# Optimization experiments

Hardware: AMD Instinct MI355X
Metric: run time of the kernel (lower is better)

## Reference

```python
import jax, jax.numpy as jnp
import numpy as np

N_NODES = 100000
N_EDGES = 1600000
D = 128


def setup_inputs() -> dict:
    key = jax.random.key(0)
    ks = jax.random.split(key, 8)
    x = jax.random.normal(ks[0], (N_NODES, D), dtype=jnp.float32)
    edge_index = jax.random.randint(ks[1], (2, N_EDGES), 0, N_NODES, dtype=jnp.int64)
    # Linear weights ~ fan-in scaled init
    scale = 1.0 / np.sqrt(D)
    W1 = jax.random.normal(ks[2], (D, D), dtype=jnp.float32) * scale
    W2 = jax.random.normal(ks[3], (D, D), dtype=jnp.float32) * scale
    W3 = jax.random.normal(ks[4], (D, D), dtype=jnp.float32) * scale
    b1 = jnp.zeros((D,), jnp.float32)
    b2 = jnp.zeros((D,), jnp.float32)
    b3 = jnp.zeros((D,), jnp.float32)
    # train_eps=True, PyG initializes eps to 0
    eps1 = jnp.zeros((), jnp.float32)
    eps2 = jnp.zeros((), jnp.float32)
    eps3 = jnp.zeros((), jnp.float32)
    return {"x": x, "edge_index": edge_index,
            "W1": W1, "b1": b1, "eps1": eps1,
            "W2": W2, "b2": b2, "eps2": eps2,
            "W3": W3, "b3": b3, "eps3": eps3}


def _gin_conv(x, src, dst, eps, W, b):
    # scatter-add neighbor aggregation: sum_{j in N(i)} x_j
    agg = jax.ops.segment_sum(x[src], dst, num_segments=N_NODES)  # [N, D]
    h = (1.0 + eps) * x + agg
    return jax.nn.relu(h @ W + b)


def reference(x, edge_index, W1, b1, eps1, W2, b2, eps2, W3, b3, eps3):
    src, dst = edge_index[0], edge_index[1]
    h = _gin_conv(x, src, dst, eps1, W1, b1)   # conv1 (dropout p=0 -> identity)
    h = _gin_conv(h, src, dst, eps2, W2, b2)
    h = _gin_conv(h, src, dst, eps3, W3, b3)
    return jax.nn.log_softmax(h, axis=1)
```

## Files before the change

### kernel.cpp

```cpp
#include <hip/hip_runtime.h>
#include <hip/hip_bf16.h>

#define N_NODES 100000
#define N_EDGES 1600000
#define D 128
#define NRANGE 8
#define RANGE_SZ 12500
#define SB_PER_RANGE 196
#define NBUCKET (NRANGE * SB_PER_RANGE)
#define G_PART 512
#define CH_PART 3125
#define G_DEG 128
#define CH_DEG 784
#define G_X2B 12500
#define PLANE ((size_t)N_NODES * 64)

typedef __attribute__((ext_vector_type(8))) short bf16x8;
typedef __attribute__((ext_vector_type(8))) unsigned short u16x8;
typedef __attribute__((ext_vector_type(4))) float f32x4;
typedef unsigned int u32;

__device__ inline ushort f2b(float x) {
    union { float f; unsigned u; } v; v.f = x;
    unsigned r = (v.u + 0x7fff + ((v.u >> 16) & 1)) >> 16;
    return (ushort)r;
}
__device__ inline float b2f(ushort b) {
    union { unsigned u; float f; } v; v.u = ((unsigned)b) << 16;
    return v.f;
}

__global__ void prep_kernel(const float* __restrict__ x, ushort* __restrict__ xb,
                            const int* __restrict__ dst, int* __restrict__ bhist1,
                            const float* __restrict__ W1, const float* __restrict__ W2,
                            const float* __restrict__ W3,
                            ushort* __restrict__ wt_hi, ushort* __restrict__ wt_lo) {
    __shared__ int lh[NRANGE];
    int b = blockIdx.x;
    if (b < G_X2B) {
        int i = b * 256 + threadIdx.x;
        if (i < N_NODES * D / 4) {
            float4 v = ((const float4*)x)[i];
            ushort4 o;
            o.x = f2b(v.x); o.y = f2b(v.y); o.z = f2b(v.z); o.w = f2b(v.w);
            int node = i >> 5;
            int f0 = (i & 31) * 4;
            int plane = f0 >> 6;
            *(ushort4*)(xb + plane * PLANE + (size_t)node * 64 + (f0 & 63)) = o;
        }
    } else if (b < G_X2B + G_PART) {
        int blk = b - G_X2B;
        if (threadIdx.x < NRANGE) lh[threadIdx.x] = 0;
        __syncthreads();
        int s0 = blk * CH_PART, s1 = s0 + CH_PART;
        if (s1 > N_EDGES) s1 = N_EDGES;
        for (int i = s0 + threadIdx.x; i < s1; i += 256)
            atomicAdd(&lh[dst[i] / RANGE_SZ], 1);
        __syncthreads();
        if (threadIdx.x < NRANGE) bhist1[blk * NRANGE + threadIdx.x] = lh[threadIdx.x];
    } else {
        int blk = b - G_X2B - G_PART;
        int layer = blk >> 6;
        int t = (blk & 63) * 256 + threadIdx.x;
        const float* W = layer == 0 ? W1 : layer == 1 ? W2 : W3;
        int k = t >> 7, n = t & 127;
        float w = W[t];
        ushort hi = f2b(w);
        ushort lo = f2b(w - b2f(hi));
        wt_hi[layer * D * D + n * D + k] = hi;
        wt_lo[layer * D * D + n * D + k] = lo;
    }
}


__global__ void scan1_kernel(const int* __restrict__ bhist1, int* __restrict__ cbase1,
                             int* __restrict__ rs) {
    int r = threadIdx.x >> 6, lane = threadIdx.x & 63;
    __shared__ int rtot[NRANGE], roff[NRANGE];
    int excl[8];
    int run = 0;
    #pragma unroll
    for (int seg = 0; seg < 8; ++seg) {
        int b = seg * 64 + lane;
        int v = bhist1[b * NRANGE + r];
        int sc = v;
        #pragma unroll
        for (int off = 1; off < 64; off <<= 1) {
            int y = __shfl_up(sc, off);
            if (lane >= off) sc += y;
        }
        excl[seg] = run + sc - v;
        run += __shfl(sc, 63);
    }
    if (lane == 63) rtot[r] = run;
    __syncthreads();
    if (threadIdx.x == 0) {
        int a = 0;
        for (int i = 0; i < NRANGE; ++i) { roff[i] = a; a += rtot[i]; }
    }
    __syncthreads();
    int base = roff[r];
    #pragma unroll
    for (int seg = 0; seg < 8; ++seg)
        cbase1[(seg * 64 + lane) * NRANGE + r] = base + excl[seg];
    if (threadIdx.x < NRANGE) rs[threadIdx.x] = roff[threadIdx.x];
    if (threadIdx.x == 0) rs[NRANGE] = N_EDGES;
}

__global__ void place1_kernel(const int* __restrict__ src, const int* __restrict__ dst,
                              const int* __restrict__ cbase1, u32* __restrict__ epack1) {
    __shared__ int cur[NRANGE];
    if (threadIdx.x < NRANGE) cur[threadIdx.x] = cbase1[blockIdx.x * NRANGE + threadIdx.x];
    __syncthreads();
    int s0 = blockIdx.x * CH_PART, s1 = s0 + CH_PART;
    if (s1 > N_EDGES) s1 = N_EDGES;
    for (int i = s0 + threadIdx.x; i < s1; i += 256) {
        int d = dst[i], s = src[i];
        int r = d / RANGE_SZ;
        int dl = d - r * RANGE_SZ;
        int p = atomicAdd(&cur[r], 1);
        epack1[p] = ((u32)dl << 17) | (u32)s;
    }
}

__global__ void hist2_kernel(const u32* __restrict__ epack1, const int* __restrict__ rs,
                             int* __restrict__ bhist2) {
    __shared__ int lh[SB_PER_RANGE];
    for (int i = threadIdx.x; i < SB_PER_RANGE; i += 256) lh[i] = 0;
    __syncthreads();
    int r = blockIdx.x >> 6, j = blockIdx.x & 63;
    int e0 = rs[r], e1 = rs[r + 1];
    int cs = (e1 - e0 + 63) >> 6;
    int s0 = e0 + j * cs, s1 = s0 + cs;
    if (s1 > e1) s1 = e1;
    for (int i = s0 + threadIdx.x; i < s1; i += 256)
        atomicAdd(&lh[epack1[i] >> 23], 1);
    __syncthreads();
    for (int i = threadIdx.x; i < SB_PER_RANGE; i += 256)
        bhist2[blockIdx.x * SB_PER_RANGE + i] = lh[i];
}

__global__ void scan2_kernel(const int* __restrict__ bhist2, const int* __restrict__ rs,
                             int* __restrict__ cbase2, int* __restrict__ bucket_start) {
    int r = blockIdx.x;
    __shared__ int tot[SB_PER_RANGE];
    __shared__ int base[SB_PER_RANGE];
    int sb = threadIdx.x;
    if (sb < SB_PER_RANGE) {
        int s = 0;
        for (int j = 0; j < 64; ++j) s += bhist2[(r * 64 + j) * SB_PER_RANGE + sb];
        tot[sb] = s;
    }
    __syncthreads();
    if (threadIdx.x == 0) {
        int a = 0;
        for (int i = 0; i < SB_PER_RANGE; ++i) { base[i] = a; a += tot[i]; }
    }
    __syncthreads();
    if (sb < SB_PER_RANGE) {
        int run = rs[r] + base[sb];
        bucket_start[r * SB_PER_RANGE + sb] = run;
        for (int j = 0; j < 64; ++j) {
            cbase2[(r * 64 + j) * SB_PER_RANGE + sb] = run;
            run += bhist2[(r * 64 + j) * SB_PER_RANGE + sb];
        }
    }
    if (r == NRANGE - 1 && threadIdx.x == 0) bucket_start[NBUCKET] = N_EDGES;
}

__global__ void place2_kernel(const u32* __restrict__ epack1, const int* __restrict__ rs,
                              const int* __restrict__ cbase2, u32* __restrict__ epack2) {
    __shared__ int cur[SB_PER_RANGE];
    for (int i = threadIdx.x; i < SB_PER_RANGE; i += 256)
        cur[i] = cbase2[blockIdx.x * SB_PER_RANGE + i];
    __syncthreads();
    int r = blockIdx.x >> 6, j = blockIdx.x & 63;
    int e0 = rs[r], e1 = rs[r + 1];
    int cs = (e1 - e0 + 63) >> 6;
    int s0 = e0 + j * cs, s1 = s0 + cs;
    if (s1 > e1) s1 = e1;
    for (int i = s0 + threadIdx.x; i < s1; i += 256) {
        u32 e = epack1[i];
        int sb = e >> 23;
        int p = atomicAdd(&cur[sb], 1);
        epack2[p] = e & 0x7FFFFFu;
    }
}

__global__ void sort3_kernel(const u32* __restrict__ epack2, const int* __restrict__ bucket_start,
                             int* __restrict__ row_ptr, int* __restrict__ col,
                             int* __restrict__ deg) {
    int b = blockIdx.x;
    int r = b / SB_PER_RANGE, sb = b - r * SB_PER_RANGE;
    int node_base = r * RANGE_SZ + sb * 64;
    int nb = r * RANGE_SZ + RANGE_SZ - node_base;
    if (nb > 64) nb = 64;
    int e0 = bucket_start[b], e1 = bucket_start[b + 1];
    __shared__ int hist[64], cur[64];
    if (threadIdx.x < 64) hist[threadIdx.x] = 0;
    __syncthreads();
    for (int i = e0 + threadIdx.x; i < e1; i += 256)
        atomicAdd(&hist[(epack2[i] >> 17) & 63], 1);
    __syncthreads();
    if (threadIdx.x < 64) {
        int v = hist[threadIdx.x];
        int sc = v;
        #pragma unroll
        for (int off = 1; off < 64; off <<= 1) {
            int y = __shfl_up(sc, off);
            if (threadIdx.x >= off) sc += y;
        }
        int ex = e0 + sc - v;
        cur[threadIdx.x] = ex;
        if (threadIdx.x < nb) {
            row_ptr[node_base + threadIdx.x] = ex;
            deg[node_base + threadIdx.x] = v;
        }
    }
    __syncthreads();
    for (int i = e0 + threadIdx.x; i < e1; i += 256) {
        u32 e = epack2[i];
        int l = (e >> 17) & 63;
        int p = atomicAdd(&cur[l], 1);
        col[p] = (int)(e & 0x1FFFFu);
    }
    if (b == NBUCKET - 1 && threadIdx.x == 0) row_ptr[N_NODES] = N_EDGES;
}


__global__ void deghist_kernel(const int* __restrict__ deg, int* __restrict__ bdh) {
    __shared__ int lh[128];
    if (threadIdx.x < 128) lh[threadIdx.x] = 0;
    __syncthreads();
    int s0 = blockIdx.x * CH_DEG, s1 = s0 + CH_DEG;
    if (s1 > N_NODES) s1 = N_NODES;
    for (int i = s0 + threadIdx.x; i < s1; i += 256)
        atomicAdd(&lh[min(deg[i], 127)], 1);
    __syncthreads();
    if (threadIdx.x < 128) bdh[blockIdx.x * 128 + threadIdx.x] = lh[threadIdx.x];
}

__global__ void degscan_kernel(const int* __restrict__ bdh, int* __restrict__ cbdeg) {
    __shared__ int sh[128];
    int t = threadIdx.x;
    int tot = 0;
    for (int j = 0; j < G_DEG; ++j) tot += bdh[j * 128 + t];
    sh[t] = tot;
    __syncthreads();
    if (t == 0) {
        int run = 0;
        for (int b = 127; b >= 0; --b) { int c = sh[b]; sh[b] = run; run += c; }
    }
    __syncthreads();
    int run = sh[t];
    for (int j = 0; j < G_DEG; ++j) {
        cbdeg[j * 128 + t] = run;
        run += bdh[j * 128 + t];
    }
}

__global__ void degplace_kernel(const int* __restrict__ deg, const int* __restrict__ cbdeg,
                                int* __restrict__ perm) {
    __shared__ int cur[128];
    if (threadIdx.x < 128) cur[threadIdx.x] = cbdeg[blockIdx.x * 128 + threadIdx.x];
    __syncthreads();
    int s0 = blockIdx.x * CH_DEG, s1 = s0 + CH_DEG;
    if (s1 > N_NODES) s1 = N_NODES;
    for (int i = s0 + threadIdx.x; i < s1; i += 256) {
        int p = atomicAdd(&cur[min(deg[i], 127)], 1);
        perm[p] = i;
    }
}


__global__ void aggregate_kernel(const ushort* __restrict__ xb, const int* __restrict__ row_ptr,
                                 const int* __restrict__ col, const int* __restrict__ perm,
                                 const float* __restrict__ eps_p, ushort* __restrict__ hb) {
    int plane = blockIdx.x & 1;
    int task = threadIdx.x >> 3;
    int l8 = threadIdx.x & 7;
    int qidx = (blockIdx.x >> 1) * 32 + task;
    if (qidx >= N_NODES) return;
    int node = perm[qidx];
    const ushort* xp = xb + plane * PLANE;
    int beg = row_ptr[node], end = row_ptr[node + 1];
    float a0[8] = {0,0,0,0,0,0,0,0};
    float a1[8] = {0,0,0,0,0,0,0,0};
    int e = beg;
    for (; e + 7 < end; e += 8) {
        int s[8];
        #pragma unroll
        for (int j = 0; j < 8; ++j) s[j] = col[e + j];
        u16x8 v[8];
        #pragma unroll
        for (int j = 0; j < 8; ++j)
            v[j] = *(const u16x8*)(xp + ((size_t)s[j] << 6) + l8 * 8);
        #pragma unroll
        for (int j = 0; j < 8; ++j) {
            float* a = (j & 1) ? a1 : a0;
            #pragma unroll
            for (int k = 0; k < 8; ++k) a[k] += b2f(v[j][k]);
        }
    }
    if (e + 3 < end) {
        int s[4];
        #pragma unroll
        for (int j = 0; j < 4; ++j) s[j] = col[e + j];
        u16x8 v[4];
        #pragma unroll
        for (int j = 0; j < 4; ++j)
            v[j] = *(const u16x8*)(xp + ((size_t)s[j] << 6) + l8 * 8);
        #pragma unroll
        for (int j = 0; j < 4; ++j) {
            float* a = (j & 1) ? a1 : a0;
            #pragma unroll
            for (int k = 0; k < 8; ++k) a[k] += b2f(v[j][k]);
        }
        e += 4;
    }
    for (; e < end; ++e) {
        int s = col[e];
        u16x8 v = *(const u16x8*)(xp + ((size_t)s << 6) + l8 * 8);
        #pragma unroll
        for (int k = 0; k < 8; ++k) a0[k] += b2f(v[k]);
    }
    float scale = 1.0f + *eps_p;
    u16x8 xi = *(const u16x8*)(xp + ((size_t)node << 6) + l8 * 8);
    u16x8 ho;
    #pragma unroll
    for (int k = 0; k < 8; ++k) {
        float o = a0[k] + a1[k] + scale * b2f(xi[k]);
        ho[k] = f2b(o);
    }
    *(u16x8*)(hb + plane * PLANE + ((size_t)node << 6) + l8 * 8) = ho;
}

template <int MODE>
__launch_bounds__(256, 2)
__global__ void gemm_relu_mfma(const ushort* __restrict__ hb,
                               const ushort* __restrict__ wt_hi, const ushort* __restrict__ wt_lo,
                               const float* __restrict__ bias,
                               float* __restrict__ outf, ushort* __restrict__ outb) {
    int wv = threadIdx.x >> 6, lane = threadIdx.x & 63;
    int r0 = blockIdx.x * 128 + wv * 32;
    int arow = lane & 15, agrp = lane >> 4;
    bf16x8 Ah[2][4];
    #pragma unroll
    for (int mf = 0; mf < 2; ++mf) {
        int row = r0 + mf * 16 + arow;
        size_t rb0 = (size_t)row << 6;
        #pragma unroll
        for (int kf = 0; kf < 4; ++kf) {
            size_t off = (kf < 2) ? rb0 + kf * 32 + agrp * 8
                                  : PLANE + rb0 + (kf - 2) * 32 + agrp * 8;
            Ah[mf][kf] = *(const bf16x8*)(hb + off);
        }
    }
    f32x4 acc[2][8];
    #pragma unroll
    for (int mf = 0; mf < 2; ++mf)
        #pragma unroll
        for (int nf = 0; nf < 8; ++nf)
            acc[mf][nf] = (f32x4){0.f, 0.f, 0.f, 0.f};
    #pragma unroll
    for (int nf = 0; nf < 8; ++nf) {
        #pragma unroll
        for (int kf = 0; kf < 4; ++kf) {
            size_t wb = (size_t)(nf * 16 + arow) * D + kf * 32 + agrp * 8;
            bf16x8 bh = *(const bf16x8*)(wt_hi + wb);
            bf16x8 bl = *(const bf16x8*)(wt_lo + wb);
            #pragma unroll
            for (int mf = 0; mf < 2; ++mf) {
                acc[mf][nf] = __builtin_amdgcn_mfma_f32_16x16x32_bf16(Ah[mf][kf], bh, acc[mf][nf], 0, 0, 0);
                acc[mf][nf] = __builtin_amdgcn_mfma_f32_16x16x32_bf16(Ah[mf][kf], bl, acc[mf][nf], 0, 0, 0);
            }
        }
    }
    float bcol[8];
    #pragma unroll
    for (int nf = 0; nf < 8; ++nf) bcol[nf] = bias[nf * 16 + arow];
    if (MODE == 0) {
        int crow = agrp * 4;
        #pragma unroll
        for (int mf = 0; mf < 2; ++mf) {
            #pragma unroll
            for (int nf = 0; nf < 8; ++nf) {
                int coln = nf * 16 + arow;
                size_t pbase = (nf >> 2) ? PLANE : 0;
                #pragma unroll
                for (int r = 0; r < 4; ++r) {
                    int row = r0 + mf * 16 + crow + r;
                    if (row < N_NODES)
                        outb[pbase + ((size_t)row << 6) + (coln & 63)] =
                            f2b(fmaxf(acc[mf][nf][r] + bcol[nf], 0.f));
                }
            }
        }
    } else {
        #pragma unroll
        for (int mf = 0; mf < 2; ++mf) {
            #pragma unroll
            for (int rr = 0; rr < 4; ++rr) {
                float v[8];
                #pragma unroll
                for (int nf = 0; nf < 8; ++nf)
                    v[nf] = fmaxf(acc[mf][nf][rr] + bcol[nf], 0.f);
                float m = v[0];
                #pragma unroll
                for (int nf = 1; nf < 8; ++nf) m = fmaxf(m, v[nf]);
                #pragma unroll
                for (int off = 1; off < 16; off <<= 1) m = fmaxf(m, __shfl_xor(m, off));
                float s = 0.f;
                #pragma unroll
                for (int nf = 0; nf < 8; ++nf) s += __expf(v[nf] - m);
                #pragma unroll
                for (int off = 1; off < 16; off <<= 1) s += __shfl_xor(s, off);
                float lse = m + __logf(s);
                int row = r0 + mf * 16 + agrp * 4 + rr;
                if (row < N_NODES) {
                    #pragma unroll
                    for (int nf = 0; nf < 8; ++nf)
                        outf[(size_t)row * D + nf * 16 + arow] = v[nf] - lse;
                }
            }
        }
    }
}

extern "C" void kernel_launch(void* const* d_in, const int* in_sizes, int n_in,
                              void* d_out, int out_size, void* d_ws, size_t ws_size,
                              hipStream_t stream) {
    (void)in_sizes; (void)n_in; (void)out_size; (void)ws_size;
    const float* x  = (const float*)d_in[0];
    const int*   ei = (const int*)d_in[1];
    const int*   src = ei;
    const int*   dst = ei + N_EDGES;
    const float* W1 = (const float*)d_in[2];
    const float* b1 = (const float*)d_in[3];
    const float* e1 = (const float*)d_in[4];
    const float* W2 = (const float*)d_in[5];
    const float* b2 = (const float*)d_in[6];
    const float* e2 = (const float*)d_in[7];
    const float* W3 = (const float*)d_in[8];
    const float* b3 = (const float*)d_in[9];
    const float* e3 = (const float*)d_in[10];
    float* out = (float*)d_out;

    char* ws = (char*)d_ws;
    int*    rs           = (int*)ws;
    int*    bucket_start = (int*)(ws + 1024);
    int*    bhist1       = (int*)(ws + 8192);
    int*    cbase1       = (int*)(ws + 24576);
    int*    bhist2       = (int*)(ws + 40960);
    int*    cbase2       = (int*)(ws + 442368);
    int*    row_ptr      = (int*)(ws + 851968);
    int*    deg          = (int*)(ws + 1253376);
    int*    perm         = (int*)(ws + 1654784);
    int*    bdh          = (int*)(ws + 2055168);
    int*    cbdeg        = (int*)(ws + 2120704);
    int*    col          = (int*)(ws + 2193408);
    ushort* wt_hi        = (ushort*)(ws + 8650752);
    ushort* wt_lo        = (ushort*)(ws + 8749056);
    ushort* xb           = (ushort*)(ws + 9437184);
    ushort* hb           = (ushort*)(ws + 35651584);
    u32*    epack1       = (u32*)(ws + 35651584);
    u32*    epack2       = (u32*)(ws + 42991616);

    prep_kernel<<<G_X2B + G_PART + 192, 256, 0, stream>>>(x, xb, dst, bhist1,
                                                          W1, W2, W3, wt_hi, wt_lo);

    scan1_kernel<<<1, 512, 0, stream>>>(bhist1, cbase1, rs);
    place1_kernel<<<G_PART, 256, 0, stream>>>(src, dst, cbase1, epack1);
    hist2_kernel<<<G_PART, 256, 0, stream>>>(epack1, rs, bhist2);
    scan2_kernel<<<NRANGE, 256, 0, stream>>>(bhist2, rs, cbase2, bucket_start);
    place2_kernel<<<G_PART, 256, 0, stream>>>(epack1, rs, cbase2, epack2);
    sort3_kernel<<<NBUCKET, 256, 0, stream>>>(epack2, bucket_start, row_ptr, col, deg);

    deghist_kernel<<<G_DEG, 256, 0, stream>>>(deg, bdh);
    degscan_kernel<<<1, 128, 0, stream>>>(bdh, cbdeg);
    degplace_kernel<<<G_DEG, 256, 0, stream>>>(deg, cbdeg, perm);

    const int aggGrid = 2 * ((N_NODES + 31) / 32);
    const int gemmGrid = (N_NODES + 127) / 128;

    aggregate_kernel<<<aggGrid, 256, 0, stream>>>(xb, row_ptr, col, perm, e1, hb);
    gemm_relu_mfma<0><<<gemmGrid, 256, 0, stream>>>(hb, wt_hi, wt_lo, b1, nullptr, xb);
    aggregate_kernel<<<aggGrid, 256, 0, stream>>>(xb, row_ptr, col, perm, e2, hb);
    gemm_relu_mfma<0><<<gemmGrid, 256, 0, stream>>>(hb, wt_hi + D * D, wt_lo + D * D, b2, nullptr, xb);
    aggregate_kernel<<<aggGrid, 256, 0, stream>>>(xb, row_ptr, col, perm, e3, hb);
    gemm_relu_mfma<1><<<gemmGrid, 256, 0, stream>>>(hb, wt_hi + 2 * D * D, wt_lo + 2 * D * D, b3, out, nullptr);
}
```

Baseline: 371.1 us.

## Fuse CSR build and degree-sort kernels into one cooperative kernel

Merges the ten preprocessing kernels (bf16 conversion, weight split, two-level bucket sort to CSR, degree histogram/scan/permutation) into one cooperative kernel of 512 blocks. The stages are separated by grid.sync instead of kernel launches. The aim is to remove per-launch overhead and the idle gaps between the many small serial kernels. In exchange, the x-to-bf16 conversion now runs as a grid-stride loop over fewer blocks, and single-block scan phases leave the rest of the grid idle at each barrier.

```diff
diff --git a/kernel.cpp b/kernel.cpp
--- a/kernel.cpp
+++ b/kernel.cpp
@@ -1,5 +1,8 @@
 #include <hip/hip_runtime.h>
 #include <hip/hip_bf16.h>
+#include <hip/hip_cooperative_groups.h>
+
+namespace cg = cooperative_groups;
 
 #define N_NODES 100000
 #define N_EDGES 1600000
@@ -8,7 +11,7 @@
 #define RANGE_SZ 12500
 #define SB_PER_RANGE 196
 #define NBUCKET (NRANGE * SB_PER_RANGE)
-#define G_PART 512
+#define NB_COOP 512
 #define CH_PART 3125
 #define G_DEG 128
 #define CH_DEG 784
@@ -30,16 +33,37 @@
     return v.f;
 }
 
-__global__ void prep_kernel(const float* __restrict__ x, ushort* __restrict__ xb,
-                            const int* __restrict__ dst, int* __restrict__ bhist1,
-                            const float* __restrict__ W1, const float* __restrict__ W2,
-                            const float* __restrict__ W3,
-                            ushort* __restrict__ wt_hi, ushort* __restrict__ wt_lo) {
-    __shared__ int lh[NRANGE];
-    int b = blockIdx.x;
-    if (b < G_X2B) {
-        int i = b * 256 + threadIdx.x;
-        if (i < N_NODES * D / 4) {
+__global__ void build_kernel(const float* __restrict__ x, ushort* __restrict__ xb,
+                             const int* __restrict__ src, const int* __restrict__ dst,
+                             const float* __restrict__ W1, const float* __restrict__ W2,
+                             const float* __restrict__ W3,
+                             ushort* __restrict__ wt_hi, ushort* __restrict__ wt_lo,
+                             int* __restrict__ bhist1, int* __restrict__ cbase1,
+                             int* __restrict__ rs,
+                             int* __restrict__ bhist2, int* __restrict__ cbase2,
+                             int* __restrict__ bucket_start,
+                             u32* __restrict__ epack1, u32* __restrict__ epack2,
+                             int* __restrict__ row_ptr, int* __restrict__ col,
+                             int* __restrict__ deg,
+                             int* __restrict__ bdh, int* __restrict__ cbdeg,
+                             int* __restrict__ perm) {
+    cg::grid_group grid = cg::this_grid();
+    __shared__ int sh[512];
+    int tid = threadIdx.x;
+    int bid = blockIdx.x;
+
+    {
+        if (tid < NRANGE) sh[tid] = 0;
+        __syncthreads();
+        int s0 = bid * CH_PART, s1 = s0 + CH_PART;
+        if (s1 > N_EDGES) s1 = N_EDGES;
+        for (int i = s0 + tid; i < s1; i += 256)
+            atomicAdd(&sh[dst[i] / RANGE_SZ], 1);
+        __syncthreads();
+        if (tid < NRANGE) bhist1[bid * NRANGE + tid] = sh[tid];
+
+        for (int c = bid; c < G_X2B; c += NB_COOP) {
+            int i = c * 256 + tid;
             float4 v = ((const float4*)x)[i];
             ushort4 o;
             o.x = f2b(v.x); o.y = f2b(v.y); o.z = f2b(v.z); o.w = f2b(v.w);
@@ -48,227 +72,217 @@
             int plane = f0 >> 6;
             *(ushort4*)(xb + plane * PLANE + (size_t)node * 64 + (f0 & 63)) = o;
         }
-    } else if (b < G_X2B + G_PART) {
-        int blk = b - G_X2B;
-        if (threadIdx.x < NRANGE) lh[threadIdx.x] = 0;
-        __syncthreads();
-        int s0 = blk * CH_PART, s1 = s0 + CH_PART;
+        if (bid < 192) {
+            int layer = bid >> 6;
+            int t = (bid & 63) * 256 + tid;
+            const float* W = layer == 0 ? W1 : layer == 1 ? W2 : W3;
+            int k = t >> 7, n = t & 127;
+            float w = W[t];
+            ushort hi = f2b(w);
+            ushort lo = f2b(w - b2f(hi));
+            wt_hi[layer * D * D + n * D + k] = hi;
+            wt_lo[layer * D * D + n * D + k] = lo;
+        }
+    }
+    grid.sync();
+
+    if (bid == 0) {
+        int w = tid >> 6, lane = tid & 63;
+        int excl[2][8];
+        #pragma unroll
+        for (int rr = 0; rr < 2; ++rr) {
+            int r = w * 2 + rr;
+            int run = 0;
+            #pragma unroll
+            for (int seg = 0; seg < 8; ++seg) {
+                int b = seg * 64 + lane;
+                int v = bhist1[b * NRANGE + r];
+                int sc = v;
+                #pragma unroll
+                for (int off = 1; off < 64; off <<= 1) {
+                    int y = __shfl_up(sc, off);
+                    if (lane >= off) sc += y;
+                }
+                excl[rr][seg] = run + sc - v;
+                run += __shfl(sc, 63);
+            }
+            if (lane == 63) sh[r] = run;
+        }
+        __syncthreads();
+        if (tid == 0) {
+            int a = 0;
+            for (int i = 0; i < NRANGE; ++i) { sh[8 + i] = a; a += sh[i]; }
+        }
+        __syncthreads();
+        #pragma unroll
+        for (int rr = 0; rr < 2; ++rr) {
+            int r = w * 2 + rr;
+            int base = sh[8 + r];
+            #pragma unroll
+            for (int seg = 0; seg < 8; ++seg)
+                cbase1[(seg * 64 + lane) * NRANGE + r] = base + excl[rr][seg];
+        }
+        if (tid < NRANGE) rs[tid] = sh[8 + tid];
+        if (tid == 0) rs[NRANGE] = N_EDGES;
+    }
+    grid.sync();
+
+    {
+        if (tid < NRANGE) sh[tid] = cbase1[bid * NRANGE + tid];
+        __syncthreads();
+        int s0 = bid * CH_PART, s1 = s0 + CH_PART;
         if (s1 > N_EDGES) s1 = N_EDGES;
-        for (int i = s0 + threadIdx.x; i < s1; i += 256)
-            atomicAdd(&lh[dst[i] / RANGE_SZ], 1);
-        __syncthreads();
-        if (threadIdx.x < NRANGE) bhist1[blk * NRANGE + threadIdx.x] = lh[threadIdx.x];
-    } else {
-        int blk = b - G_X2B - G_PART;
-        int layer = blk >> 6;
-        int t = (blk & 63) * 256 + threadIdx.x;
-        const float* W = layer == 0 ? W1 : layer == 1 ? W2 : W3;
-        int k = t >> 7, n = t & 127;
-        float w = W[t];
-        ushort hi = f2b(w);
-        ushort lo = f2b(w - b2f(hi));
-        wt_hi[layer * D * D + n * D + k] = hi;
-        wt_lo[layer * D * D + n * D + k] = lo;
-    }
-}
-
-
-__global__ void scan1_kernel(const int* __restrict__ bhist1, int* __restrict__ cbase1,
-                             int* __restrict__ rs) {
-    int r = threadIdx.x >> 6, lane = threadIdx.x & 63;
-    __shared__ int rtot[NRANGE], roff[NRANGE];
-    int excl[8];
-    int run = 0;
-    #pragma unroll
-    for (int seg = 0; seg < 8; ++seg) {
-        int b = seg * 64 + lane;
-        int v = bhist1[b * NRANGE + r];
-        int sc = v;
-        #pragma unroll
-        for (int off = 1; off < 64; off <<= 1) {
-            int y = __shfl_up(sc, off);
-            if (lane >= off) sc += y;
-        }
-        excl[seg] = run + sc - v;
-        run += __shfl(sc, 63);
-    }
-    if (lane == 63) rtot[r] = run;
-    __syncthreads();
-    if (threadIdx.x == 0) {
-        int a = 0;
-        for (int i = 0; i < NRANGE; ++i) { roff[i] = a; a += rtot[i]; }
-    }
-    __syncthreads();
-    int base = roff[r];
-    #pragma unroll
-    for (int seg = 0; seg < 8; ++seg)
-        cbase1[(seg * 64 + lane) * NRANGE + r] = base + excl[seg];
-    if (threadIdx.x < NRANGE) rs[threadIdx.x] = roff[threadIdx.x];
-    if (threadIdx.x == 0) rs[NRANGE] = N_EDGES;
-}
-
-__global__ void place1_kernel(const int* __restrict__ src, const int* __restrict__ dst,
-                              const int* __restrict__ cbase1, u32* __restrict__ epack1) {
-    __shared__ int cur[NRANGE];
-    if (threadIdx.x < NRANGE) cur[threadIdx.x] = cbase1[blockIdx.x * NRANGE + threadIdx.x];
-    __syncthreads();
-    int s0 = blockIdx.x * CH_PART, s1 = s0 + CH_PART;
-    if (s1 > N_EDGES) s1 = N_EDGES;
-    for (int i = s0 + threadIdx.x; i < s1; i += 256) {
-        int d = dst[i], s = src[i];
-        int r = d / RANGE_SZ;
-        int dl = d - r * RANGE_SZ;
-        int p = atomicAdd(&cur[r], 1);
-        epack1[p] = ((u32)dl << 17) | (u32)s;
-    }
-}
-
-__global__ void hist2_kernel(const u32* __restrict__ epack1, const int* __restrict__ rs,
-                             int* __restrict__ bhist2) {
-    __shared__ int lh[SB_PER_RANGE];
-    for (int i = threadIdx.x; i < SB_PER_RANGE; i += 256) lh[i] = 0;
-    __syncthreads();
-    int r = blockIdx.x >> 6, j = blockIdx.x & 63;
-    int e0 = rs[r], e1 = rs[r + 1];
-    int cs = (e1 - e0 + 63) >> 6;
-    int s0 = e0 + j * cs, s1 = s0 + cs;
-    if (s1 > e1) s1 = e1;
-    for (int i = s0 + threadIdx.x; i < s1; i += 256)
-        atomicAdd(&lh[epack1[i] >> 23], 1);
-    __syncthreads();
-    for (int i = threadIdx.x; i < SB_PER_RANGE; i += 256)
-        bhist2[blockIdx.x * SB_PER_RANGE + i] = lh[i];
-}
-
-__global__ void scan2_kernel(const int* __restrict__ bhist2, const int* __restrict__ rs,
-                             int* __restrict__ cbase2, int* __restrict__ bucket_start) {
-    int r = blockIdx.x;
-    __shared__ int tot[SB_PER_RANGE];
-    __shared__ int base[SB_PER_RANGE];
-    int sb = threadIdx.x;
-    if (sb < SB_PER_RANGE) {
-        int s = 0;
-        for (int j = 0; j < 64; ++j) s += bhist2[(r * 64 + j) * SB_PER_RANGE + sb];
-        tot[sb] = s;
-    }
-    __syncthreads();
-    if (threadIdx.x == 0) {
-        int a = 0;
-        for (int i = 0; i < SB_PER_RANGE; ++i) { base[i] = a; a += tot[i]; }
-    }
-    __syncthreads();
-    if (sb < SB_PER_RANGE) {
-        int run = rs[r] + base[sb];
-        bucket_start[r * SB_PER_RANGE + sb] = run;
-        for (int j = 0; j < 64; ++j) {
-            cbase2[(r * 64 + j) * SB_PER_RANGE + sb] = run;
-            run += bhist2[(r * 64 + j) * SB_PER_RANGE + sb];
-        }
-    }
-    if (r == NRANGE - 1 && threadIdx.x == 0) bucket_start[NBUCKET] = N_EDGES;
-}
-
-__global__ void place2_kernel(const u32* __restrict__ epack1, const int* __restrict__ rs,
-                              const int* __restrict__ cbase2, u32* __restrict__ epack2) {
-    __shared__ int cur[SB_PER_RANGE];
-    for (int i = threadIdx.x; i < SB_PER_RANGE; i += 256)
-        cur[i] = cbase2[blockIdx.x * SB_PER_RANGE + i];
-    __syncthreads();
-    int r = blockIdx.x >> 6, j = blockIdx.x & 63;
-    int e0 = rs[r], e1 = rs[r + 1];
-    int cs = (e1 - e0 + 63) >> 6;
-    int s0 = e0 + j * cs, s1 = s0 + cs;
-    if (s1 > e1) s1 = e1;
-    for (int i = s0 + threadIdx.x; i < s1; i += 256) {
-        u32 e = epack1[i];
-        int sb = e >> 23;
-        int p = atomicAdd(&cur[sb], 1);
-        epack2[p] = e & 0x7FFFFFu;
-    }
-}
-
-__global__ void sort3_kernel(const u32* __restrict__ epack2, const int* __restrict__ bucket_start,
-                             int* __restrict__ row_ptr, int* __restrict__ col,
-                             int* __restrict__ deg) {
-    int b = blockIdx.x;
-    int r = b / SB_PER_RANGE, sb = b - r * SB_PER_RANGE;
-    int node_base = r * RANGE_SZ + sb * 64;
-    int nb = r * RANGE_SZ + RANGE_SZ - node_base;
-    if (nb > 64) nb = 64;
-    int e0 = bucket_start[b], e1 = bucket_start[b + 1];
-    __shared__ int hist[64], cur[64];
-    if (threadIdx.x < 64) hist[threadIdx.x] = 0;
-    __syncthreads();
-    for (int i = e0 + threadIdx.x; i < e1; i += 256)
-        atomicAdd(&hist[(epack2[i] >> 17) & 63], 1);
-    __syncthreads();
-    if (threadIdx.x < 64) {
-        int v = hist[threadIdx.x];
-        int sc = v;
-        #pragma unroll
-        for (int off = 1; off < 64; off <<= 1) {
-            int y = __shfl_up(sc, off);
-            if (threadIdx.x >= off) sc += y;
-        }
-        int ex = e0 + sc - v;
-        cur[threadIdx.x] = ex;
-        if (threadIdx.x < nb) {
-            row_ptr[node_base + threadIdx.x] = ex;
-            deg[node_base + threadIdx.x] = v;
-        }
-    }
-    __syncthreads();
-    for (int i = e0 + threadIdx.x; i < e1; i += 256) {
-        u32 e = epack2[i];
-        int l = (e >> 17) & 63;
-        int p = atomicAdd(&cur[l], 1);
-        col[p] = (int)(e & 0x1FFFFu);
-    }
-    if (b == NBUCKET - 1 && threadIdx.x == 0) row_ptr[N_NODES] = N_EDGES;
-}
-
-
-__global__ void deghist_kernel(const int* __restrict__ deg, int* __restrict__ bdh) {
-    __shared__ int lh[128];
-    if (threadIdx.x < 128) lh[threadIdx.x] = 0;
-    __syncthreads();
-    int s0 = blockIdx.x * CH_DEG, s1 = s0 + CH_DEG;
-    if (s1 > N_NODES) s1 = N_NODES;
-    for (int i = s0 + threadIdx.x; i < s1; i += 256)
-        atomicAdd(&lh[min(deg[i], 127)], 1);
-    __syncthreads();
-    if (threadIdx.x < 128) bdh[blockIdx.x * 128 + threadIdx.x] = lh[threadIdx.x];
-}
-
-__global__ void degscan_kernel(const int* __restrict__ bdh, int* __restrict__ cbdeg) {
-    __shared__ int sh[128];
-    int t = threadIdx.x;
-    int tot = 0;
-    for (int j = 0; j < G_DEG; ++j) tot += bdh[j * 128 + t];
-    sh[t] = tot;
-    __syncthreads();
-    if (t == 0) {
-        int run = 0;
-        for (int b = 127; b >= 0; --b) { int c = sh[b]; sh[b] = run; run += c; }
-    }
-    __syncthreads();
-    int run = sh[t];
-    for (int j = 0; j < G_DEG; ++j) {
-        cbdeg[j * 128 + t] = run;
-        run += bdh[j * 128 + t];
-    }
-}
-
-__global__ void degplace_kernel(const int* __restrict__ deg, const int* __restrict__ cbdeg,
-                                int* __restrict__ perm) {
-    __shared__ int cur[128];
-    if (threadIdx.x < 128) cur[threadIdx.x] = cbdeg[blockIdx.x * 128 + threadIdx.x];
-    __syncthreads();
-    int s0 = blockIdx.x * CH_DEG, s1 = s0 + CH_DEG;
-    if (s1 > N_NODES) s1 = N_NODES;
-    for (int i = s0 + threadIdx.x; i < s1; i += 256) {
-        int p = atomicAdd(&cur[min(deg[i], 127)], 1);
-        perm[p] = i;
+        for (int i = s0 + tid; i < s1; i += 256) {
+            int d = dst[i], s = src[i];
+            int r = d / RANGE_SZ;
+            int dl = d - r * RANGE_SZ;
+            int p = atomicAdd(&sh[r], 1);
+            epack1[p] = ((u32)dl << 17) | (u32)s;
+        }
+    }
+    grid.sync();
+
+    {
+        for (int i = tid; i < SB_PER_RANGE; i += 256) sh[i] = 0;
+        __syncthreads();
+        int r = bid >> 6, j = bid & 63;
+        int e0 = rs[r], e1 = rs[r + 1];
+        int cs = (e1 - e0 + 63) >> 6;
+        int s0 = e0 + j * cs, s1 = s0 + cs;
+        if (s1 > e1) s1 = e1;
+        for (int i = s0 + tid; i < s1; i += 256)
+            atomicAdd(&sh[epack1[i] >> 23], 1);
+        __syncthreads();
+        for (int i = tid; i < SB_PER_RANGE; i += 256)
+            bhist2[bid * SB_PER_RANGE + i] = sh[i];
+    }
+    grid.sync();
+
+    if (bid < NRANGE) {
+        int r = bid;
+        int sb = tid;
+        if (sb < SB_PER_RANGE) {
+            int s = 0;
+            for (int j = 0; j < 64; ++j) s += bhist2[(r * 64 + j) * SB_PER_RANGE + sb];
+            sh[sb] = s;
+        }
+        __syncthreads();
+        if (tid == 0) {
+            int a = 0;
+            for (int i = 0; i < SB_PER_RANGE; ++i) { sh[196 + i] = a; a += sh[i]; }
+        }
+        __syncthreads();
+        if (sb < SB_PER_RANGE) {
+            int run = rs[r] + sh[196 + sb];
+            bucket_start[r * SB_PER_RANGE + sb] = run;
+            for (int j = 0; j < 64; ++j) {
+                cbase2[(r * 64 + j) * SB_PER_RANGE + sb] = run;
+                run += bhist2[(r * 64 + j) * SB_PER_RANGE + sb];
+            }
+        }
+        if (r == NRANGE - 1 && tid == 0) bucket_start[NBUCKET] = N_EDGES;
+    }
+    grid.sync();
+
+    {
+        for (int i = tid; i < SB_PER_RANGE; i += 256)
+            sh[i] = cbase2[bid * SB_PER_RANGE + i];
+        __syncthreads();
+        int r = bid >> 6, j = bid & 63;
+        int e0 = rs[r], e1 = rs[r + 1];
+        int cs = (e1 - e0 + 63) >> 6;
+        int s0 = e0 + j * cs, s1 = s0 + cs;
+        if (s1 > e1) s1 = e1;
+        for (int i = s0 + tid; i < s1; i += 256) {
+            u32 e = epack1[i];
+            int sb = e >> 23;
+            int p = atomicAdd(&sh[sb], 1);
+            epack2[p] = e & 0x7FFFFFu;
+        }
+    }
+    grid.sync();
+
+    for (int b = bid; b < NBUCKET; b += NB_COOP) {
+        int r = b / SB_PER_RANGE, sb = b - r * SB_PER_RANGE;
+        int node_base = r * RANGE_SZ + sb * 64;
+        int nb = r * RANGE_SZ + RANGE_SZ - node_base;
+        if (nb > 64) nb = 64;
+        int e0 = bucket_start[b], e1 = bucket_start[b + 1];
+        if (tid < 64) sh[tid] = 0;
+        __syncthreads();
+        for (int i = e0 + tid; i < e1; i += 256)
+            atomicAdd(&sh[(epack2[i] >> 17) & 63], 1);
+        __syncthreads();
+        if (tid < 64) {
+            int v = sh[tid];
+            int sc = v;
+            #pragma unroll
+            for (int off = 1; off < 64; off <<= 1) {
+                int y = __shfl_up(sc, off);
+                if (tid >= off) sc += y;
+            }
+            int ex = e0 + sc - v;
+            sh[64 + tid] = ex;
+            if (tid < nb) {
+                row_ptr[node_base + tid] = ex;
+                deg[node_base + tid] = v;
+            }
+        }
+        __syncthreads();
+        for (int i = e0 + tid; i < e1; i += 256) {
+            u32 e = epack2[i];
+            int l = (e >> 17) & 63;
+            int p = atomicAdd(&sh[64 + l], 1);
+            col[p] = (int)(e & 0x1FFFFu);
+        }
+        if (b == NBUCKET - 1 && tid == 0) row_ptr[N_NODES] = N_EDGES;
+        __syncthreads();
+    }
+    grid.sync();
+
+    if (bid < G_DEG) {
+        if (tid < 128) sh[tid] = 0;
+        __syncthreads();
+        int s0 = bid * CH_DEG, s1 = s0 + CH_DEG;
+        if (s1 > N_NODES) s1 = N_NODES;
+        for (int i = s0 + tid; i < s1; i += 256)
+            atomicAdd(&sh[min(deg[i], 127)], 1);
+        __syncthreads();
+        if (tid < 128) bdh[bid * 128 + tid] = sh[tid];
+    }
+    grid.sync();
+
+    if (bid == 0) {
+        if (tid < 128) {
+            int tot = 0;
+            for (int j = 0; j < G_DEG; ++j) tot += bdh[j * 128 + tid];
+            sh[tid] = tot;
+        }
+        __syncthreads();
+        if (tid == 0) {
+            int run = 0;
+            for (int b = 127; b >= 0; --b) { int c = sh[b]; sh[b] = run; run += c; }
+        }
+        __syncthreads();
+        if (tid < 128) {
+            int run = sh[tid];
+            for (int j = 0; j < G_DEG; ++j) {
+                cbdeg[j * 128 + tid] = run;
+                run += bdh[j * 128 + tid];
+            }
+        }
+    }
+    grid.sync();
+
+    if (bid < G_DEG) {
+        if (tid < 128) sh[tid] = cbdeg[bid * 128 + tid];
+        __syncthreads();
+        int s0 = bid * CH_DEG, s1 = s0 + CH_DEG;
+        if (s1 > N_NODES) s1 = N_NODES;
+        for (int i = s0 + tid; i < s1; i += 256) {
+            int p = atomicAdd(&sh[min(deg[i], 127)], 1);
+            perm[p] = i;
+        }
     }
 }
 
@@ -466,19 +480,18 @@
     u32*    epack1       = (u32*)(ws + 35651584);
     u32*    epack2       = (u32*)(ws + 42991616);
 
-    prep_kernel<<<G_X2B + G_PART + 192, 256, 0, stream>>>(x, xb, dst, bhist1,
-                                                          W1, W2, W3, wt_hi, wt_lo);
-
-    scan1_kernel<<<1, 512, 0, stream>>>(bhist1, cbase1, rs);
-    place1_kernel<<<G_PART, 256, 0, stream>>>(src, dst, cbase1, epack1);
-    hist2_kernel<<<G_PART, 256, 0, stream>>>(epack1, rs, bhist2);
-    scan2_kernel<<<NRANGE, 256, 0, stream>>>(bhist2, rs, cbase2, bucket_start);
-    place2_kernel<<<G_PART, 256, 0, stream>>>(epack1, rs, cbase2, epack2);
-    sort3_kernel<<<NBUCKET, 256, 0, stream>>>(epack2, bucket_start, row_ptr, col, deg);
-
-    deghist_kernel<<<G_DEG, 256, 0, stream>>>(deg, bdh);
-    degscan_kernel<<<1, 128, 0, stream>>>(bdh, cbdeg);
-    degplace_kernel<<<G_DEG, 256, 0, stream>>>(deg, cbdeg, perm);
+    void* args[] = {
+        (void*)&x, (void*)&xb, (void*)&src, (void*)&dst,
+        (void*)&W1, (void*)&W2, (void*)&W3,
+        (void*)&wt_hi, (void*)&wt_lo,
+        (void*)&bhist1, (void*)&cbase1, (void*)&rs,
+        (void*)&bhist2, (void*)&cbase2, (void*)&bucket_start,
+        (void*)&epack1, (void*)&epack2,
+        (void*)&row_ptr, (void*)&col, (void*)&deg,
+        (void*)&bdh, (void*)&cbdeg, (void*)&perm
+    };
+    hipLaunchCooperativeKernel((void*)build_kernel, dim3(NB_COOP), dim3(256),
+                               args, 0, stream);
 
     const int aggGrid = 2 * ((N_NODES + 31) / 32);
     const int gemmGrid = (N_NODES + 127) / 128;
```

After: 887.6 us. 139% more time.
